# Performance work log

Hardware: AMD Instinct MI355X
Metric: run time of the kernel (lower is better)

Reference implementation:

```python
import jax, jax.numpy as jnp
import numpy as np

P = 8      # patch_size
DIM = 16   # per-head channel dim
HEADS = 4
LN_EPS = 1e-6


def _conv_patch(x, W, b):
    # stride=kernel=P patch conv; SAME degenerates to VALID when H%P==0
    y = jax.lax.conv_general_dilated(
        x, W, window_strides=(P, P), padding='VALID',
        dimension_numbers=('NHWC', 'HWIO', 'NHWC'))
    return y + b


def _proj_heads(x, W, b):
    # b h w (c p0 p1 head) -> b head (h p0) (w p1) c
    y = _conv_patch(x, W, b)
    B, hh, ww, _ = y.shape
    y = y.reshape(B, hh, ww, DIM, P, P, HEADS)
    y = y.transpose(0, 6, 1, 4, 2, 5, 3)            # b head hh p0 ww p1 c
    return y.reshape(B, HEADS, hh * P, ww * P, DIM)


def _to_patch(t):
    # n head (h p1) (w p2) c -> n head c h w p1 p2
    B, hd, H, W, c = t.shape
    t = t.reshape(B, hd, H // P, P, W // P, P, c)
    return t.transpose(0, 1, 6, 2, 4, 3, 5)


def _from_patch(t):
    # n head c h w p1 p2 -> n head (h p1) (w p2) c
    B, hd, c, hh, ww, _, _ = t.shape
    t = t.transpose(0, 1, 3, 5, 4, 6, 2)
    return t.reshape(B, hd, hh * P, ww * P, c)


def setup_inputs() -> dict:
    key = jax.random.key(0)
    ks = jax.random.split(key, 6)
    B, H, W, Cin = 4, 256, 256, 16
    feat = DIM * HEADS * P * P  # 4096
    s_qkv = 0.02
    inp = {
        'x': jax.random.normal(ks[0], (B, H, W, Cin), jnp.float32),
        'Wq': jax.random.normal(ks[1], (P, P, Cin, feat), jnp.float32) * s_qkv,
        'bq': jnp.zeros((feat,), jnp.float32),
        'Wk': jax.random.normal(ks[2], (P, P, Cin, feat), jnp.float32) * s_qkv,
        'bk': jnp.zeros((feat,), jnp.float32),
        'Wv': jax.random.normal(ks[3], (P, P, Cin, feat), jnp.float32) * s_qkv,
        'bv': jnp.zeros((feat,), jnp.float32),
        'ln_scale': jnp.ones((DIM,), jnp.float32),
        'ln_bias': jnp.zeros((DIM,), jnp.float32),
        'Wout': jax.random.normal(ks[4], (P, P, HEADS * DIM, DIM * P * P), jnp.float32) * 0.02,
        'bout': jnp.zeros((DIM * P * P,), jnp.float32),
    }
    return inp


def reference(x, Wq, bq, Wk, bk, Wv, bv, ln_scale, ln_bias, Wout, bout):
    q = _proj_heads(x, Wq, bq)  # [B, heads, H, W, dim]
    k = _proj_heads(x, Wk, bk)
    v = _proj_heads(x, Wv, bv)

    # frequency-domain 'attention': per-8x8-patch rfft2 multiply irfft2
    qf = jnp.fft.rfft2(_to_patch(q))
    kf = jnp.fft.rfft2(_to_patch(k))
    out = jnp.fft.irfft2(qf * kf, s=(P, P))
    out = _from_patch(out)                          # [B, heads, H, W, dim]

    # LayerNorm over channel dim (flax default eps=1e-6, scale+bias)
    mu = out.mean(-1, keepdims=True)
    var = ((out - mu) ** 2).mean(-1, keepdims=True)
    out = (out - mu) * jax.lax.rsqrt(var + LN_EPS) * ln_scale + ln_bias

    out = v * out
    # b head h w c -> b h w (head c)
    B, hd, H, W, c = out.shape
    out = out.transpose(0, 2, 3, 1, 4).reshape(B, H, W, hd * c)

    # output projection (no heads): conv then b h w (c p0 p1) -> b (h p0) (w p1) c
    y = _conv_patch(out, Wout, bout)
    Bo, hh, ww, _ = y.shape
    y = y.reshape(Bo, hh, ww, DIM, P, P).transpose(0, 1, 4, 2, 5, 3)
    return y.reshape(Bo, hh * P, ww * P, DIM)
```

## Files before the change

### kernel.cpp

```cpp
#include <hip/hip_runtime.h>
#include <hip/hip_bf16.h>
#include <cstdint>
#include <cstddef>

typedef float  f32x4  __attribute__((ext_vector_type(4)));
typedef __bf16 bf16x8 __attribute__((ext_vector_type(8)));
typedef __bf16 bf16x4 __attribute__((ext_vector_type(4)));


#define GLOAD_LDS16(gp, lp)                                                     \
    __builtin_amdgcn_global_load_lds(                                           \
        (const __attribute__((address_space(1))) void*)(gp),                    \
        (__attribute__((address_space(3))) void*)(lp), 16, 0, 0)

#define MFMA16(d, a, b) d = __builtin_amdgcn_mfma_f32_16x16x32_bf16(a, b, d, 0, 0, 0)

#define BAR() asm volatile("s_barrier" ::: "memory")

__global__ __launch_bounds__(256) void k_im2col(const float* __restrict__ x,
                                                __bf16* __restrict__ Xb)
{
    const int p = blockIdx.x;
    const int t = threadIdx.x;
    const int b = p >> 10, hh = (p >> 5) & 31, ww = p & 31;
    const int e = t * 4;
    const int c = e & 15, ij = e >> 4;
    const int i = ij >> 3, j = ij & 7;
    const size_t src = ((((size_t)(b * 256 + hh * 8 + i)) * 256) + (ww * 8 + j)) * 16 + c;
    f32x4 v = *(const f32x4*)(x + src);
    bf16x4 o;
    o[0] = (__bf16)v[0]; o[1] = (__bf16)v[1]; o[2] = (__bf16)v[2]; o[3] = (__bf16)v[3];
    *(bf16x4*)(Xb + (size_t)p * 1024 + e) = o;
}

__global__ __launch_bounds__(256) void k_wqkvT(const float* __restrict__ Wq,
                                               const float* __restrict__ Wk,
                                               const float* __restrict__ Wv,
                                               __bf16* __restrict__ WT)
{
    __shared__ float tile[64][261];
    int q = blockIdx.x;
    const int t = threadIdx.x;
    const int kb = q & 15;   q >>= 4;
    const int ch = q & 15;   q >>= 4;
    const int s  = q;
    const int k0 = kb * 64;
    const float* __restrict__ W = (s == 0) ? Wq : (s == 1) ? Wk : Wv;

#pragma unroll
    for (int rep = 0; rep < 16; rep++) {
        const int idx = rep * 256 + t;
        const int kl = idx >> 6, col4 = (idx & 63) * 4;
        const f32x4 v = *(const f32x4*)(W + (size_t)(k0 + kl) * 4096 + ch * 256 + col4);
        tile[kl][col4 + 0] = v[0];
        tile[kl][col4 + 1] = v[1];
        tile[kl][col4 + 2] = v[2];
        tile[kl][col4 + 3] = v[3];
    }
    __syncthreads();
    const size_t nbase = (size_t)s * 4096 + ch * 64;
#pragma unroll
    for (int rep = 0; rep < 64; rep++) {
        const int idx = rep * 256 + t;
        const int kl = idx & 63;
        const int rest = idx >> 6;
        const int p = rest & 63, h = rest >> 6;
        WT[(nbase + h * 1024 + p) * 1024 + k0 + kl] = (__bf16)tile[kl][p * 4 + h];
    }
}

__global__ __launch_bounds__(256) void k_biasperm(const float* __restrict__ bq,
                                                  const float* __restrict__ bk,
                                                  const float* __restrict__ bv,
                                                  float* __restrict__ bp)
{
    const int n = blockIdx.x * 256 + threadIdx.x;
    const int s = n >> 12;
    const int r = n & 4095;
    const int head = r >> 10, c = (r >> 6) & 15, pp = r & 63;
    const float* __restrict__ b = (s == 0) ? bq : (s == 1) ? bk : bv;
    bp[n] = b[c * 256 + pp * 4 + head];
}

__global__ __launch_bounds__(256) void k_woutT(const float* __restrict__ Wo,
                                               __bf16* __restrict__ WT)
{
    __shared__ float tile[64][129];
    const int q = blockIdx.x;
    const int t = threadIdx.x;
    const int n0 = (q & 15) * 64;
    const int k0 = (q >> 4) * 128;
    const int ch = n0 >> 6;
#pragma unroll
    for (int rep = 0; rep < 32; rep++) {
        const int idx = rep * 256 + t;
        const int kl = idx >> 6, nn = idx & 63;
        tile[nn][kl] = Wo[(size_t)(k0 + kl) * 1024 + n0 + nn];
    }
    __syncthreads();
#pragma unroll
    for (int rep = 0; rep < 32; rep++) {
        const int idx = rep * 256 + t;
        const int nn = idx >> 7, kl = idx & 127;
        const int no = ((nn >> 3) & 7) * 128 + (nn & 7) * 16 + ch;
        WT[(size_t)no * 4096 + k0 + kl] = (__bf16)tile[nn][kl];
    }
}

__device__ __forceinline__ void stage_half(const __bf16* __restrict__ mat,
                                           const int gRow0, const int K,
                                           const int k0, __bf16* lds, const int t)
{
    const int w6 = (t >> 6) << 6;
#pragma unroll
    for (int r = 0; r < 2; r++) {
        const int idx = r * 512 + t;
        const int row = idx >> 3;
        const int colb = ((t & 7) << 4) ^ ((row & 7) << 4);
        const char* gp = (const char*)(mat + (size_t)(gRow0 + row) * K + k0) + colb;
        GLOAD_LDS16(gp, (char*)lds + (size_t)(r * 512 + w6) * 16);
    }
}

__global__ __launch_bounds__(512, 1) void gemm256(const __bf16* __restrict__ A,
                                                  const __bf16* __restrict__ Bt,
                                                  __bf16* __restrict__ C,
                                                  const float* __restrict__ bias,
                                                  const int M, const int N,
                                                  const int K, const int nby)
{
    __shared__ __bf16 As[2][256 * 64];
    __shared__ __bf16 Bs[2][256 * 64];

    const int t = threadIdx.x;
    const int l = t & 63, w = t >> 6;
    const int wr = w >> 2, wc = w & 3;

    const int nwg = (int)gridDim.x, cpx = nwg >> 3;
    const int bid = (int)blockIdx.x;
    const int sbid = (bid & 7) * cpx + (bid >> 3);
    const int bm = sbid % nby, bn = sbid / nby;
    const int row0 = bm * 256, col0 = bn * 256;

    const int lrow = l & 15;
    const int lkb  = (l >> 4) << 4;
    const int lswz = (l & 7) << 4;
    const int ce0 = ((0  + lkb) ^ lswz) >> 1;
    const int ce1 = ((64 + lkb) ^ lswz) >> 1;

    const int arow = wr * 128 + lrow;
    const int brow = wc * 64 + lrow;

    const int NT = K >> 6;
    f32x4 acc[8][4] = {};
    bf16x8 a0[4][2], a1[4][2], b0[2][2], b1[2][2];

    stage_half(A,  row0,       K, 0,  As[0],        t);
    stage_half(A,  row0 + 128, K, 0,  As[0] + 8192, t);
    stage_half(A,  row0,       K, 64, As[1],        t);
    stage_half(A,  row0 + 128, K, 64, As[1] + 8192, t);
    stage_half(Bt, col0,       K, 0,  Bs[0],        t);
    stage_half(Bt, col0 + 128, K, 0,  Bs[0] + 8192, t);
    asm volatile("s_waitcnt vmcnt(0)" ::: "memory");
    BAR();
#pragma unroll
    for (int mi = 0; mi < 4; ++mi) {
        const int rr = (arow + mi * 16) * 64;
        a0[mi][0] = *(const bf16x8*)&As[0][rr + ce0];
        a0[mi][1] = *(const bf16x8*)&As[0][rr + ce1];
    }

    int cur = 0;
    for (int it = 0; it < NT; ++it) {
        const __bf16* AsC = As[cur];
        const __bf16* AsN = As[cur ^ 1];
        const __bf16* BsC = Bs[cur];
        __bf16* BsN = Bs[cur ^ 1];
        const bool stB = (it + 1 < NT);
        const bool stA = (it + 2 < NT);
        const bool pfA = (it + 1 < NT);
        const int kB = (it + 1) << 6;
        const int kA = (it + 2) << 6;

        BAR();
#pragma unroll
        for (int ni = 0; ni < 2; ++ni) {
            const int rr = (brow + ni * 16) * 64;
            b0[ni][0] = *(const bf16x8*)&BsC[rr + ce0];
            b0[ni][1] = *(const bf16x8*)&BsC[rr + ce1];
        }
#pragma unroll
        for (int ni = 0; ni < 2; ++ni) {
            const int rr = (brow + 32 + ni * 16) * 64;
            b1[ni][0] = *(const bf16x8*)&BsC[rr + ce0];
            b1[ni][1] = *(const bf16x8*)&BsC[rr + ce1];
        }
#pragma unroll
        for (int mi = 0; mi < 4; ++mi) {
            const int rr = (arow + 64 + mi * 16) * 64;
            a1[mi][0] = *(const bf16x8*)&AsC[rr + ce0];
            a1[mi][1] = *(const bf16x8*)&AsC[rr + ce1];
        }
        if (stB) stage_half(Bt, col0, K, kB, BsN, t);
        __builtin_amdgcn_s_setprio(1);
#pragma unroll
        for (int mi = 0; mi < 4; ++mi)
#pragma unroll
            for (int ni = 0; ni < 2; ++ni) {
                MFMA16(acc[mi][ni], a0[mi][0], b0[ni][0]);
                MFMA16(acc[mi][ni], a0[mi][1], b0[ni][1]);
            }
        __builtin_amdgcn_s_setprio(0);

        BAR();
        if (stB) stage_half(Bt, col0 + 128, K, kB, BsN + 8192, t);
        __builtin_amdgcn_s_setprio(1);
#pragma unroll
        for (int mi = 0; mi < 4; ++mi)
#pragma unroll
            for (int ni = 0; ni < 2; ++ni) {
                MFMA16(acc[mi][2 + ni], a0[mi][0], b1[ni][0]);
                MFMA16(acc[mi][2 + ni], a0[mi][1], b1[ni][1]);
            }
        __builtin_amdgcn_s_setprio(0);
        asm volatile("s_waitcnt vmcnt(4)" ::: "memory");

        BAR();
        if (pfA) {
#pragma unroll
            for (int mi = 0; mi < 4; ++mi) {
                const int rr = (arow + mi * 16) * 64;
                a0[mi][0] = *(const bf16x8*)&AsN[rr + ce0];
                a0[mi][1] = *(const bf16x8*)&AsN[rr + ce1];
            }
        }
        __builtin_amdgcn_s_setprio(1);
#pragma unroll
        for (int mi = 0; mi < 4; ++mi)
#pragma unroll
            for (int ni = 0; ni < 2; ++ni) {
                MFMA16(acc[4 + mi][ni], a1[mi][0], b0[ni][0]);
                MFMA16(acc[4 + mi][ni], a1[mi][1], b0[ni][1]);
            }
        __builtin_amdgcn_s_setprio(0);

        BAR();
        if (stA) {
            stage_half(A, row0,       K, kA, As[cur],        t);
            stage_half(A, row0 + 128, K, kA, As[cur] + 8192, t);
            asm volatile("s_waitcnt vmcnt(4)" ::: "memory");
        } else {
            asm volatile("s_waitcnt vmcnt(0)" ::: "memory");
        }
        __builtin_amdgcn_s_setprio(1);
#pragma unroll
        for (int mi = 0; mi < 4; ++mi)
#pragma unroll
            for (int ni = 0; ni < 2; ++ni) {
                MFMA16(acc[4 + mi][2 + ni], a1[mi][0], b1[ni][0]);
                MFMA16(acc[4 + mi][2 + ni], a1[mi][1], b1[ni][1]);
            }
        __builtin_amdgcn_s_setprio(0);

        cur ^= 1;
    }

    const int rbase = row0 + wr * 128;
    const int cbase = col0 + wc * 64;
    const int jr = (l >> 4) * 4;
#pragma unroll
    for (int m = 0; m < 8; ++m)
#pragma unroll
        for (int n = 0; n < 4; ++n) {
            const int cw = cbase + n * 16 + lrow;
            const float bsv = bias[cw];
#pragma unroll
            for (int j = 0; j < 4; ++j) {
                const int rw = rbase + m * 16 + jr + j;
                C[(size_t)rw * N + cw] = (__bf16)(acc[m][n][j] + bsv);
            }
        }
}

template <int BN, int EPI>
__global__ __launch_bounds__(256, 3) void gemm_glds(const __bf16* __restrict__ A,
                                                    const __bf16* __restrict__ Bt,
                                                    void* __restrict__ Cout,
                                                    const float* __restrict__ bias,
                                                    const int M, const int N,
                                                    const int K, const int nbx)
{
    constexpr int BM  = 128, BK = 64;
    constexpr int NF  = BN / 32;
    constexpr int APW = (BM * BK / 512) / 4;
    constexpr int BPW = (BN * BK / 512) / 4;
    __shared__ __bf16 As[BM * BK];
    __shared__ __bf16 Bs[BN * BK];

    const int t = threadIdx.x;
    const int l = t & 63, w = t >> 6;

    const int nwg  = (int)gridDim.x;
    const int cpx  = nwg >> 3;
    const int bid  = (int)blockIdx.x;
    const int sbid = (bid & 7) * cpx + (bid >> 3);
    const int bm = sbid / nbx, bn = sbid - bm * nbx;
    const int row0 = bm * BM, col0 = bn * BN;

    const int wr = w >> 1, wc = w & 1;
    const int lr = l & 15;
    const int lk = (l >> 4) * 8;
    const int srow = l >> 3;
    const int scol = (l & 7) * 8;

    f32x4 acc[4][NF] = {};

    for (int k0 = 0; k0 < K; k0 += BK) {
        __syncthreads();
#pragma unroll
        for (int p = 0; p < APW; p++) {
            const int chunk = w * APW + p;
            const __bf16* gp = A + (size_t)(row0 + chunk * 8 + srow) * K + k0 + scol;
            GLOAD_LDS16(gp, &As[chunk * 512]);
        }
#pragma unroll
        for (int p = 0; p < BPW; p++) {
            const int chunk = w * BPW + p;
            const __bf16* gp = Bt + (size_t)(col0 + chunk * 8 + srow) * K + k0 + scol;
            GLOAD_LDS16(gp, &Bs[chunk * 512]);
        }
        __syncthreads();
#pragma unroll
        for (int kk = 0; kk < 2; kk++) {
            bf16x8 af[4], bfr[NF];
#pragma unroll
            for (int m = 0; m < 4; m++)
                af[m] = *(const bf16x8*)&As[(wr * 64 + m * 16 + lr) * BK + kk * 32 + lk];
#pragma unroll
            for (int n = 0; n < NF; n++)
                bfr[n] = *(const bf16x8*)&Bs[(wc * (BN / 2) + n * 16 + lr) * BK + kk * 32 + lk];
#pragma unroll
            for (int m = 0; m < 4; m++)
#pragma unroll
                for (int n = 0; n < NF; n++)
                    acc[m][n] = __builtin_amdgcn_mfma_f32_16x16x32_bf16(
                        af[m], bfr[n], acc[m][n], 0, 0, 0);
        }
    }

    const int rbase = row0 + wr * 64;
    const int cbase = col0 + wc * (BN / 2);
    if (EPI == 0) {
        __bf16* __restrict__ C = (__bf16*)Cout;
#pragma unroll
        for (int m = 0; m < 4; m++)
#pragma unroll
            for (int n = 0; n < NF; n++) {
                const int cw = cbase + n * 16 + lr;
                const float bsv = bias[cw];
#pragma unroll
                for (int j = 0; j < 4; j++) {
                    const int rw = rbase + m * 16 + (l >> 4) * 4 + j;
                    C[(size_t)rw * N + cw] = (__bf16)(acc[m][n][j] + bsv);
                }
            }
    } else {
        float* __restrict__ Y = (float*)Cout;
#pragma unroll
        for (int m = 0; m < 4; m++)
#pragma unroll
            for (int n = 0; n < NF; n++) {
                const int cw = cbase + n * 16 + lr;
                const float bsv = bias[((cw & 15) << 6) + ((cw >> 7) << 3) + ((cw >> 4) & 7)];
                const int p0 = cw >> 7, low = cw & 127;
#pragma unroll
                for (int j = 0; j < 4; j++) {
                    const int rw = rbase + m * 16 + (l >> 4) * 4 + j;
                    const int b = rw >> 10, hh = (rw >> 5) & 31, wwp = rw & 31;
                    const size_t addr =
                        (size_t)(b * 256 + hh * 8 + p0) * 4096 + wwp * 128 + low;
                    Y[addr] = acc[m][n][j] + bsv;
                }
            }
    }
}

__global__ __launch_bounds__(128) void k_freqconv(const __bf16* __restrict__ C1,
                                                  const float* __restrict__ lns,
                                                  const float* __restrict__ lnb,
                                                  __bf16* __restrict__ Z)
{
    const int blk = blockIdx.x;
    const int p = blk >> 2, head = blk & 3;
    const int t = threadIdx.x;

    __shared__ float qs[16 * 68];
    __shared__ float ks[16 * 68];
    __shared__ float vs[16 * 68];
    __shared__ float os[16 * 68];

    const __bf16* __restrict__ base = C1 + (size_t)p * 12288 + head * 1024;
    {
        const int cl = t >> 3, off = (t & 7) * 8;
        const bf16x8 vq = *(const bf16x8*)(base + cl * 64 + off);
        const bf16x8 vk = *(const bf16x8*)(base + 4096 + cl * 64 + off);
        const bf16x8 vv = *(const bf16x8*)(base + 8192 + cl * 64 + off);
#pragma unroll
        for (int e = 0; e < 8; e++) {
            qs[cl * 68 + off + e] = (float)vq[e];
            ks[cl * 68 + off + e] = (float)vk[e];
            vs[cl * 68 + off + e] = (float)vv[e];
        }
    }
    __syncthreads();

    const int cc = t >> 3, p0 = t & 7;
    float outr[8] = {0.f, 0.f, 0.f, 0.f, 0.f, 0.f, 0.f, 0.f};
#pragma unroll
    for (int i0 = 0; i0 < 8; i0++) {
        const int kr = (p0 - i0) & 7;
        const f32x4 qa = *(const f32x4*)&qs[cc * 68 + i0 * 8];
        const f32x4 qb = *(const f32x4*)&qs[cc * 68 + i0 * 8 + 4];
        const f32x4 ka = *(const f32x4*)&ks[cc * 68 + kr * 8];
        const f32x4 kb = *(const f32x4*)&ks[cc * 68 + kr * 8 + 4];
        const float qrow[8] = {qa[0], qa[1], qa[2], qa[3], qb[0], qb[1], qb[2], qb[3]};
        const float krow[8] = {ka[0], ka[1], ka[2], ka[3], kb[0], kb[1], kb[2], kb[3]};
#pragma unroll
        for (int j = 0; j < 8; j++) {
            const float qv = qrow[j];
#pragma unroll
            for (int p1 = 0; p1 < 8; p1++)
                outr[p1] = fmaf(qv, krow[(p1 - j) & 7], outr[p1]);
        }
    }
#pragma unroll
    for (int e = 0; e < 8; e++)
        os[cc * 68 + p0 * 8 + e] = outr[e];
    __syncthreads();

    if (t < 64) {
        const int pp = t;
        float o[16];
        float mu = 0.f;
#pragma unroll
        for (int c2 = 0; c2 < 16; c2++) { o[c2] = os[c2 * 68 + pp]; mu += o[c2]; }
        mu *= 0.0625f;
        float var = 0.f;
#pragma unroll
        for (int c2 = 0; c2 < 16; c2++) { const float d = o[c2] - mu; var = fmaf(d, d, var); }
        var *= 0.0625f;
        const float rs = rsqrtf(var + 1e-6f);
        bf16x8 z0, z1;
#pragma unroll
        for (int c2 = 0; c2 < 16; c2++) {
            float zv = (o[c2] - mu) * rs * lns[c2] + lnb[c2];
            zv *= vs[c2 * 68 + pp];
            if (c2 < 8) z0[c2] = (__bf16)zv; else z1[c2 - 8] = (__bf16)zv;
        }
        bf16x8* zp = (bf16x8*)(Z + (size_t)p * 4096 + pp * 64 + head * 16);
        zp[0] = z0;
        zp[1] = z1;
    }
}

extern "C" void kernel_launch(void* const* d_in, const int* in_sizes, int n_in,
                              void* d_out, int out_size, void* d_ws, size_t ws_size,
                              hipStream_t stream)
{
    const float* x   = (const float*)d_in[0];
    const float* Wq  = (const float*)d_in[1];
    const float* bq  = (const float*)d_in[2];
    const float* Wk  = (const float*)d_in[3];
    const float* bk  = (const float*)d_in[4];
    const float* Wv  = (const float*)d_in[5];
    const float* bv  = (const float*)d_in[6];
    const float* lns = (const float*)d_in[7];
    const float* lnb = (const float*)d_in[8];
    const float* Wo  = (const float*)d_in[9];
    const float* bo  = (const float*)d_in[10];
    float* out = (float*)d_out;

    char* ws = (char*)d_ws;
    __bf16* Xb    = (__bf16*)(ws);
    __bf16* WqkvT = (__bf16*)(ws + 8388608);
    float*  bperm = (float*) (ws + 33554432);
    __bf16* WoutT = (__bf16*)(ws + 33603584);
    __bf16* C1    = (__bf16*)(ws + 41992192);
    __bf16* Z     = (__bf16*)(ws + 142655488);

    k_im2col  <<<dim3(4096), dim3(256), 0, stream>>>(x, Xb);
    k_wqkvT   <<<dim3(768),  dim3(256), 0, stream>>>(Wq, Wk, Wv, WqkvT);
    k_biasperm<<<dim3(48),   dim3(256), 0, stream>>>(bq, bk, bv, bperm);
    k_woutT   <<<dim3(512),  dim3(256), 0, stream>>>(Wo, WoutT);

    gemm256<<<dim3(768), dim3(512), 0, stream>>>(Xb, WqkvT, C1, bperm,
                                                 4096, 12288, 1024, 16);

    k_freqconv<<<dim3(16384), dim3(128), 0, stream>>>(C1, lns, lnb, Z);

    gemm_glds<128, 1><<<dim3(256), dim3(256), 0, stream>>>(Z, WoutT, (void*)out, bo,
                                                           4096, 1024, 4096, 8);
}
```

Baseline: 251.5 us.

## Issue A-tile prefetch earlier in gemm256 and retile output GEMM to BN64/BK128

In the big QKV GEMM, the next A-tile global-to-LDS loads are now issued in the second phase of each iteration instead of the fourth. The vmcnt waits are reorganized to match, so the loads have more MFMA work to hide behind. The output-projection GEMM is templated on BK and launched with BN=64, BK=128 and 512 workgroups. This doubles the grid for better CU coverage and halves the number of k-iterations and barriers. The cost is lower occupancy (launch bounds 3 to 2) and risky hand-tuned waitcnt accounting.

```diff
diff --git a/kernel.cpp b/kernel.cpp
--- a/kernel.cpp
+++ b/kernel.cpp
@@ -214,6 +214,10 @@
 
         BAR();
         if (stB) stage_half(Bt, col0 + 128, K, kB, BsN + 8192, t);
+        if (stA) {
+            stage_half(A, row0,       K, kA, As[cur],        t);
+            stage_half(A, row0 + 128, K, kA, As[cur] + 8192, t);
+        }
         __builtin_amdgcn_s_setprio(1);
 #pragma unroll
         for (int mi = 0; mi < 4; ++mi)
@@ -223,7 +227,10 @@
                 MFMA16(acc[mi][2 + ni], a0[mi][1], b1[ni][1]);
             }
         __builtin_amdgcn_s_setprio(0);
-        asm volatile("s_waitcnt vmcnt(4)" ::: "memory");
+        if (pfA) {
+            if (stA) asm volatile("s_waitcnt vmcnt(8)" ::: "memory");
+            else     asm volatile("s_waitcnt vmcnt(4)" ::: "memory");
+        }
 
         BAR();
         if (pfA) {
@@ -245,13 +252,6 @@
         __builtin_amdgcn_s_setprio(0);
 
         BAR();
-        if (stA) {
-            stage_half(A, row0,       K, kA, As[cur],        t);
-            stage_half(A, row0 + 128, K, kA, As[cur] + 8192, t);
-            asm volatile("s_waitcnt vmcnt(4)" ::: "memory");
-        } else {
-            asm volatile("s_waitcnt vmcnt(0)" ::: "memory");
-        }
         __builtin_amdgcn_s_setprio(1);
 #pragma unroll
         for (int mi = 0; mi < 4; ++mi)
@@ -261,6 +261,10 @@
                 MFMA16(acc[4 + mi][2 + ni], a1[mi][1], b1[ni][1]);
             }
         __builtin_amdgcn_s_setprio(0);
+        if (stB) {
+            if (stA) asm volatile("s_waitcnt vmcnt(4)" ::: "memory");
+            else     asm volatile("s_waitcnt vmcnt(0)" ::: "memory");
+        }
 
         cur ^= 1;
     }
@@ -282,16 +286,18 @@
         }
 }
 
-template <int BN, int EPI>
-__global__ __launch_bounds__(256, 3) void gemm_glds(const __bf16* __restrict__ A,
+template <int BN, int BK, int EPI>
+__global__ __launch_bounds__(256, 2) void gemm_glds(const __bf16* __restrict__ A,
                                                     const __bf16* __restrict__ Bt,
                                                     void* __restrict__ Cout,
                                                     const float* __restrict__ bias,
                                                     const int M, const int N,
                                                     const int K, const int nbx)
 {
-    constexpr int BM  = 128, BK = 64;
+    constexpr int BM  = 128;
     constexpr int NF  = BN / 32;
+    constexpr int CPR = BK / 8;
+    constexpr int RPC = 512 / BK;
     constexpr int APW = (BM * BK / 512) / 4;
     constexpr int BPW = (BN * BK / 512) / 4;
     __shared__ __bf16 As[BM * BK];
@@ -310,8 +316,8 @@
     const int wr = w >> 1, wc = w & 1;
     const int lr = l & 15;
     const int lk = (l >> 4) * 8;
-    const int srow = l >> 3;
-    const int scol = (l & 7) * 8;
+    const int srow = l / CPR;
+    const int scol = (l % CPR) * 8;
 
     f32x4 acc[4][NF] = {};
 
@@ -320,18 +326,18 @@
 #pragma unroll
         for (int p = 0; p < APW; p++) {
             const int chunk = w * APW + p;
-            const __bf16* gp = A + (size_t)(row0 + chunk * 8 + srow) * K + k0 + scol;
+            const __bf16* gp = A + (size_t)(row0 + chunk * RPC + srow) * K + k0 + scol;
             GLOAD_LDS16(gp, &As[chunk * 512]);
         }
 #pragma unroll
         for (int p = 0; p < BPW; p++) {
             const int chunk = w * BPW + p;
-            const __bf16* gp = Bt + (size_t)(col0 + chunk * 8 + srow) * K + k0 + scol;
+            const __bf16* gp = Bt + (size_t)(col0 + chunk * RPC + srow) * K + k0 + scol;
             GLOAD_LDS16(gp, &Bs[chunk * 512]);
         }
         __syncthreads();
 #pragma unroll
-        for (int kk = 0; kk < 2; kk++) {
+        for (int kk = 0; kk < BK / 32; kk++) {
             bf16x8 af[4], bfr[NF];
 #pragma unroll
             for (int m = 0; m < 4; m++)
@@ -498,6 +504,6 @@
 
     k_freqconv<<<dim3(16384), dim3(128), 0, stream>>>(C1, lns, lnb, Z);
 
-    gemm_glds<128, 1><<<dim3(256), dim3(256), 0, stream>>>(Z, WoutT, (void*)out, bo,
-                                                           4096, 1024, 4096, 8);
-}
+    gemm_glds<64, 128, 1><<<dim3(512), dim3(256), 0, stream>>>(Z, WoutT, (void*)out, bo,
+                                                               4096, 1024, 4096, 16);
+}
```

Measured after the change: 273.6 us. 8.8% more time.

## Split-K the output projection GEMM and add a reduce-scatter kernel

Applied to the files above, without the earlier changes.

The final GEMM (M=4096, N=1024, K=4096) launched only 256 workgroups, so it is split into two K halves with 512 workgroups. Each writes fp32 partials into workspace that reuses the C1 region. A new elementwise kernel sums the two partials, adds the permuted bias and performs the output scatter with vectorised stores. This buys more parallelism on a many-CU GPU at the cost of 32 MB of extra partial traffic and one more kernel launch.

```diff
diff --git a/kernel.cpp b/kernel.cpp
--- a/kernel.cpp
+++ b/kernel.cpp
@@ -282,13 +282,11 @@
         }
 }
 
-template <int BN, int EPI>
-__global__ __launch_bounds__(256, 3) void gemm_glds(const __bf16* __restrict__ A,
-                                                    const __bf16* __restrict__ Bt,
-                                                    void* __restrict__ Cout,
-                                                    const float* __restrict__ bias,
-                                                    const int M, const int N,
-                                                    const int K, const int nbx)
+template <int BN>
+__global__ __launch_bounds__(256, 3) void gemm_splitk(const __bf16* __restrict__ A,
+                                                      const __bf16* __restrict__ Bt,
+                                                      float* __restrict__ Pout,
+                                                      const int K, const int kc)
 {
     constexpr int BM  = 128, BK = 64;
     constexpr int NF  = BN / 32;
@@ -304,8 +302,11 @@
     const int cpx  = nwg >> 3;
     const int bid  = (int)blockIdx.x;
     const int sbid = (bid & 7) * cpx + (bid >> 3);
-    const int bm = sbid / nbx, bn = sbid - bm * nbx;
+    const int bm = sbid >> 4;
+    const int ks = (sbid >> 3) & 1;
+    const int bn = sbid & 7;
     const int row0 = bm * BM, col0 = bn * BN;
+    const int kstart = ks * kc;
 
     const int wr = w >> 1, wc = w & 1;
     const int lr = l & 15;
@@ -315,7 +316,7 @@
 
     f32x4 acc[4][NF] = {};
 
-    for (int k0 = 0; k0 < K; k0 += BK) {
+    for (int k0 = kstart; k0 < kstart + kc; k0 += BK) {
         __syncthreads();
 #pragma unroll
         for (int p = 0; p < APW; p++) {
@@ -348,41 +349,40 @@
         }
     }
 
+    float* __restrict__ P = Pout + (size_t)ks * 4194304;
     const int rbase = row0 + wr * 64;
     const int cbase = col0 + wc * (BN / 2);
-    if (EPI == 0) {
-        __bf16* __restrict__ C = (__bf16*)Cout;
-#pragma unroll
-        for (int m = 0; m < 4; m++)
-#pragma unroll
-            for (int n = 0; n < NF; n++) {
-                const int cw = cbase + n * 16 + lr;
-                const float bsv = bias[cw];
-#pragma unroll
-                for (int j = 0; j < 4; j++) {
-                    const int rw = rbase + m * 16 + (l >> 4) * 4 + j;
-                    C[(size_t)rw * N + cw] = (__bf16)(acc[m][n][j] + bsv);
-                }
-            }
-    } else {
-        float* __restrict__ Y = (float*)Cout;
-#pragma unroll
-        for (int m = 0; m < 4; m++)
-#pragma unroll
-            for (int n = 0; n < NF; n++) {
-                const int cw = cbase + n * 16 + lr;
-                const float bsv = bias[((cw & 15) << 6) + ((cw >> 7) << 3) + ((cw >> 4) & 7)];
-                const int p0 = cw >> 7, low = cw & 127;
-#pragma unroll
-                for (int j = 0; j < 4; j++) {
-                    const int rw = rbase + m * 16 + (l >> 4) * 4 + j;
-                    const int b = rw >> 10, hh = (rw >> 5) & 31, wwp = rw & 31;
-                    const size_t addr =
-                        (size_t)(b * 256 + hh * 8 + p0) * 4096 + wwp * 128 + low;
-                    Y[addr] = acc[m][n][j] + bsv;
-                }
-            }
-    }
+#pragma unroll
+    for (int m = 0; m < 4; m++)
+#pragma unroll
+        for (int n = 0; n < NF; n++) {
+            const int cw = cbase + n * 16 + lr;
+#pragma unroll
+            for (int j = 0; j < 4; j++) {
+                const int rw = rbase + m * 16 + (l >> 4) * 4 + j;
+                P[(size_t)rw * 1024 + cw] = acc[m][n][j];
+            }
+        }
+}
+
+__global__ __launch_bounds__(256) void k_redscatter(const float* __restrict__ P,
+                                                    const float* __restrict__ bo,
+                                                    float* __restrict__ Y)
+{
+    const int i = (blockIdx.x * 256 + threadIdx.x) * 4;
+    const int rw = i >> 10, cw = i & 1023;
+    const f32x4 v0 = *(const f32x4*)(P + i);
+    const f32x4 v1 = *(const f32x4*)(P + 4194304 + i);
+    const int p0 = cw >> 7, low = cw & 127;
+    const int b = rw >> 10, hh = (rw >> 5) & 31, wwp = rw & 31;
+    float* dst = Y + (size_t)(b * 256 + hh * 8 + p0) * 4096 + wwp * 128 + low;
+    f32x4 o;
+#pragma unroll
+    for (int j = 0; j < 4; j++) {
+        const int c = cw + j;
+        o[j] = v0[j] + v1[j] + bo[((c & 15) << 6) + ((c >> 7) << 3) + ((c >> 4) & 7)];
+    }
+    *(f32x4*)dst = o;
 }
 
 __global__ __launch_bounds__(128) void k_freqconv(const __bf16* __restrict__ C1,
@@ -487,6 +487,7 @@
     __bf16* WoutT = (__bf16*)(ws + 33603584);
     __bf16* C1    = (__bf16*)(ws + 41992192);
     __bf16* Z     = (__bf16*)(ws + 142655488);
+    float*  Ppart = (float*) (ws + 41992192);
 
     k_im2col  <<<dim3(4096), dim3(256), 0, stream>>>(x, Xb);
     k_wqkvT   <<<dim3(768),  dim3(256), 0, stream>>>(Wq, Wk, Wv, WqkvT);
@@ -498,6 +499,8 @@
 
     k_freqconv<<<dim3(16384), dim3(128), 0, stream>>>(C1, lns, lnb, Z);
 
-    gemm_glds<128, 1><<<dim3(256), dim3(256), 0, stream>>>(Z, WoutT, (void*)out, bo,
-                                                           4096, 1024, 4096, 8);
-}
+    gemm_splitk<128><<<dim3(512), dim3(256), 0, stream>>>(Z, WoutT, Ppart,
+                                                          4096, 2048);
+
+    k_redscatter<<<dim3(4096), dim3(256), 0, stream>>>(Ppart, bo, out);
+}
```

New measurement: 232.4 us. 7.6% less time.
